# Performance work log

Hardware: AMD Instinct MI355X
Metric: run time of the kernel (lower is better)

Reference implementation:

```python
import jax, jax.numpy as jnp
import numpy as np
import hashlib, struct

TABLE_SIZE = 4_194_304
K_DIM = 8
BATCH = 131_072


def _sha_indices(residues_np: np.ndarray, salt: bytes, table_size: int) -> np.ndarray:
    # Faithful to HeritableTrustVault._hash: clamp, *100, int16 bytes, sha256(salt+bytes),
    # little-endian uint64 of first 8 digest bytes, mod table_size.
    q = (np.clip(residues_np, -30000.0, 30000.0) * 100.0).astype(np.int16)
    out = np.empty(q.shape[0], dtype=np.int64)
    for i in range(q.shape[0]):
        d = hashlib.sha256(salt + q[i].tobytes()).digest()
        out[i] = struct.unpack_from('<Q', d)[0] % table_size
    return out


def setup_inputs() -> dict:
    key = jax.random.key(0)
    k0, k1, k2, k3 = jax.random.split(key, 4)
    residues = jax.random.normal(k0, (BATCH, K_DIM), dtype=jnp.float32)
    survivorship = jax.random.uniform(k1, (BATCH,), dtype=jnp.float32)
    trust_table = jax.random.normal(k2, (TABLE_SIZE, K_DIM), dtype=jnp.float32)
    trust_scores = jax.random.uniform(k3, (TABLE_SIZE,), dtype=jnp.float32)
    longevity = jnp.zeros((TABLE_SIZE,), dtype=jnp.int32)
    salt = np.random.RandomState(0).randint(0, 256, 16, dtype=np.uint8).tobytes()
    indices = jnp.asarray(_sha_indices(np.asarray(residues), salt, TABLE_SIZE))
    return {
        'residues': residues,
        'survivorship': survivorship,
        'trust_table': trust_table,
        'trust_scores': trust_scores,
        'longevity': longevity,
        'indices': indices,
    }


def reference(residues, survivorship, trust_table, trust_scores, longevity, indices):
    # update(): serial compare-exchange loop semantics, vectorized.
    # Final score per slot = max(old_score, max survivorship hashing to it).
    # Winner row per slot = FIRST row with survivorship strictly > old score and
    # equal to the final score (strict '>' means later ties never overwrite).
    B = residues.shape[0]
    T = trust_scores.shape[0]
    old_at = trust_scores[indices]                                  # [B]
    new_scores = trust_scores.at[indices].max(survivorship)         # [T]
    final_at = new_scores[indices]                                  # [B]
    win = (survivorship > old_at) & (survivorship >= final_at)      # [B]
    rows = jnp.arange(B, dtype=jnp.int32)
    cand = jnp.where(win, rows, B)                                  # sentinel B = no winner
    min_row = jnp.full((T,), B, dtype=jnp.int32).at[indices].min(cand)
    has_winner = min_row < B                                        # [T]
    safe_row = jnp.where(has_winner, min_row, 0)
    new_table = jnp.where(has_winner[:, None], residues[safe_row], trust_table)
    new_longevity = longevity.at[indices].add(1)
    # query() after update
    query_scores = new_scores[indices]                              # [B]
    return query_scores, new_table, new_scores, new_longevity
```

## Files before the change

### kernel.cpp

```cpp
#include <hip/hip_runtime.h>

#define T_SIZE 4194304
#define B_SIZE 131072
#define KD 8

__global__ void vault_init_kernel(const float* __restrict__ trust_scores,
                                  const int* __restrict__ longevity,
                                  float* __restrict__ new_scores,
                                  float* __restrict__ new_longevity,
                                  int* __restrict__ min_row) {
    int t = blockIdx.x * blockDim.x + threadIdx.x;
    if (t < T_SIZE / 4) {
        float4 s = ((const float4*)trust_scores)[t];
        int4 l = ((const int4*)longevity)[t];
        float4 lf = make_float4((float)l.x, (float)l.y, (float)l.z, (float)l.w);
        ((float4*)new_scores)[t] = s;
        ((float4*)new_longevity)[t] = lf;
        ((int4*)min_row)[t] = make_int4(B_SIZE, B_SIZE, B_SIZE, B_SIZE);
    }
}

__global__ void vault_scatter_kernel(const float* __restrict__ survivorship,
                                     const int* __restrict__ indices,
                                     float* __restrict__ new_scores,
                                     float* __restrict__ new_longevity) {
    int i = blockIdx.x * blockDim.x + threadIdx.x;
    if (i < B_SIZE) {
        int idx = indices[i];
        atomicMax((int*)(new_scores + idx), __float_as_int(survivorship[i]));
        atomicAdd(new_longevity + idx, 1.0f);
    }
}

__global__ void vault_winner_kernel(const float* __restrict__ survivorship,
                                    const int* __restrict__ indices,
                                    const float* __restrict__ trust_scores,
                                    const float* __restrict__ new_scores,
                                    float* __restrict__ query_scores,
                                    int* __restrict__ min_row) {
    int i = blockIdx.x * blockDim.x + threadIdx.x;
    if (i < B_SIZE) {
        int idx = indices[i];
        float s = survivorship[i];
        float oldv = trust_scores[idx];
        float finalv = new_scores[idx];
        query_scores[i] = finalv;
        if (s > oldv && s >= finalv) {
            atomicMin(min_row + idx, i);
        }
    }
}

__global__ void vault_table_kernel(const float* __restrict__ residues,
                                   const float* __restrict__ trust_table,
                                   const int* __restrict__ min_row,
                                   float* __restrict__ new_table) {
    int t = blockIdx.x * blockDim.x + threadIdx.x;
    if (t < T_SIZE) {
        int r = min_row[t];
        const float4* src = (r < B_SIZE)
            ? (const float4*)(residues + (size_t)r * KD)
            : (const float4*)(trust_table + (size_t)t * KD);
        float4 a = src[0];
        float4 b = src[1];
        float4* dst = (float4*)(new_table + (size_t)t * KD);
        dst[0] = a;
        dst[1] = b;
    }
}

extern "C" void kernel_launch(void* const* d_in, const int* in_sizes, int n_in,
                              void* d_out, int out_size, void* d_ws, size_t ws_size,
                              hipStream_t stream) {
    const float* residues      = (const float*)d_in[0];
    const float* survivorship  = (const float*)d_in[1];
    const float* trust_table   = (const float*)d_in[2];
    const float* trust_scores  = (const float*)d_in[3];
    const int*   longevity     = (const int*)d_in[4];
    const int*   indices       = (const int*)d_in[5];

    float* query_scores  = (float*)d_out;
    float* new_table     = query_scores + B_SIZE;
    float* new_scores    = new_table + (size_t)T_SIZE * KD;
    float* new_longevity = new_scores + T_SIZE;

    int* min_row = (int*)d_ws;

    const int blk = 256;

    vault_init_kernel<<<(T_SIZE / 4 + blk - 1) / blk, blk, 0, stream>>>(
        trust_scores, longevity, new_scores, new_longevity, min_row);

    vault_scatter_kernel<<<(B_SIZE + blk - 1) / blk, blk, 0, stream>>>(
        survivorship, indices, new_scores, new_longevity);

    vault_winner_kernel<<<(B_SIZE + blk - 1) / blk, blk, 0, stream>>>(
        survivorship, indices, trust_scores, new_scores, query_scores, min_row);

    vault_table_kernel<<<(T_SIZE + blk - 1) / blk, blk, 0, stream>>>(
        residues, trust_table, min_row, new_table);
}
```

Before: 320.5 us.

## Pack score and row into a 64-bit atomicMax and fuse finalize kernels

Replaces the separate max-score scatter and min-row winner pass with a single 64-bit atomicMax per row. The key packs the score bits in the high word and the inverted row index in the low word, so the first row holding the max score wins ties. The winner pass and table-copy pass are merged into one finalize kernel that also writes new_scores and query_scores, which removes one launch and one read-modify pass over the slot arrays. The cost is a 32 MB packed workspace in place of a 16 MB min_row buffer. Correctness relies on survivorship being non-negative, so the float bits order like unsigned integers, and on zero-initialised packed words never beating the old score.

```diff
diff --git a/kernel.cpp b/kernel.cpp
--- a/kernel.cpp
+++ b/kernel.cpp
@@ -3,69 +3,67 @@
 #define T_SIZE 4194304
 #define B_SIZE 131072
 #define KD 8
+#define ROW_BLOCKS (B_SIZE / 256)
+#define SLOT_BLOCKS (T_SIZE / 256)
 
-__global__ void vault_init_kernel(const float* __restrict__ trust_scores,
-                                  const int* __restrict__ longevity,
-                                  float* __restrict__ new_scores,
+typedef unsigned long long u64;
+typedef unsigned int u32;
+
+__global__ void vault_init_kernel(const int* __restrict__ longevity,
                                   float* __restrict__ new_longevity,
-                                  int* __restrict__ min_row) {
+                                  u64* __restrict__ packed) {
     int t = blockIdx.x * blockDim.x + threadIdx.x;
-    if (t < T_SIZE / 4) {
-        float4 s = ((const float4*)trust_scores)[t];
-        int4 l = ((const int4*)longevity)[t];
-        float4 lf = make_float4((float)l.x, (float)l.y, (float)l.z, (float)l.w);
-        ((float4*)new_scores)[t] = s;
-        ((float4*)new_longevity)[t] = lf;
-        ((int4*)min_row)[t] = make_int4(B_SIZE, B_SIZE, B_SIZE, B_SIZE);
-    }
+    ulonglong2 z = {0ull, 0ull};
+    ((ulonglong2*)packed)[2 * t]     = z;
+    ((ulonglong2*)packed)[2 * t + 1] = z;
+    int4 l = ((const int4*)longevity)[t];
+    ((float4*)new_longevity)[t] =
+        make_float4((float)l.x, (float)l.y, (float)l.z, (float)l.w);
 }
 
 __global__ void vault_scatter_kernel(const float* __restrict__ survivorship,
                                      const int* __restrict__ indices,
-                                     float* __restrict__ new_scores,
+                                     u64* __restrict__ packed,
                                      float* __restrict__ new_longevity) {
     int i = blockIdx.x * blockDim.x + threadIdx.x;
-    if (i < B_SIZE) {
-        int idx = indices[i];
-        atomicMax((int*)(new_scores + idx), __float_as_int(survivorship[i]));
-        atomicAdd(new_longevity + idx, 1.0f);
-    }
+    int idx = indices[i];
+    u32 bits = __float_as_uint(survivorship[i]);
+    u64 p = ((u64)bits << 32) | (u64)(~(u32)i);
+    atomicMax(packed + idx, p);
+    atomicAdd(new_longevity + idx, 1.0f);
 }
 
-__global__ void vault_winner_kernel(const float* __restrict__ survivorship,
-                                    const int* __restrict__ indices,
-                                    const float* __restrict__ trust_scores,
-                                    const float* __restrict__ new_scores,
-                                    float* __restrict__ query_scores,
-                                    int* __restrict__ min_row) {
-    int i = blockIdx.x * blockDim.x + threadIdx.x;
-    if (i < B_SIZE) {
+__global__ void vault_finalize_kernel(const float* __restrict__ residues,
+                                      const float* __restrict__ trust_table,
+                                      const float* __restrict__ trust_scores,
+                                      const int* __restrict__ indices,
+                                      const u64* __restrict__ packed,
+                                      float* __restrict__ query_scores,
+                                      float* __restrict__ new_table,
+                                      float* __restrict__ new_scores) {
+    int b = blockIdx.x;
+    if (b < ROW_BLOCKS) {
+        int i = b * 256 + threadIdx.x;
         int idx = indices[i];
-        float s = survivorship[i];
+        u64 p = packed[idx];
+        float ms = __uint_as_float((u32)(p >> 32));
         float oldv = trust_scores[idx];
-        float finalv = new_scores[idx];
-        query_scores[i] = finalv;
-        if (s > oldv && s >= finalv) {
-            atomicMin(min_row + idx, i);
-        }
-    }
-}
-
-__global__ void vault_table_kernel(const float* __restrict__ residues,
-                                   const float* __restrict__ trust_table,
-                                   const int* __restrict__ min_row,
-                                   float* __restrict__ new_table) {
-    int t = blockIdx.x * blockDim.x + threadIdx.x;
-    if (t < T_SIZE) {
-        int r = min_row[t];
-        const float4* src = (r < B_SIZE)
+        query_scores[i] = fmaxf(oldv, ms);
+    } else {
+        int t = (b - ROW_BLOCKS) * 256 + threadIdx.x;
+        u64 p = packed[t];
+        float ms = __uint_as_float((u32)(p >> 32));
+        float oldv = trust_scores[t];
+        new_scores[t] = fmaxf(oldv, ms);
+        int r = (int)(~(u32)p);
+        const float4* src = (ms > oldv)
             ? (const float4*)(residues + (size_t)r * KD)
             : (const float4*)(trust_table + (size_t)t * KD);
         float4 a = src[0];
-        float4 b = src[1];
+        float4 c = src[1];
         float4* dst = (float4*)(new_table + (size_t)t * KD);
         dst[0] = a;
-        dst[1] = b;
+        dst[1] = c;
     }
 }
 
@@ -84,19 +82,17 @@
     float* new_scores    = new_table + (size_t)T_SIZE * KD;
     float* new_longevity = new_scores + T_SIZE;
 
-    int* min_row = (int*)d_ws;
+    u64* packed = (u64*)d_ws;
 
     const int blk = 256;
 
-    vault_init_kernel<<<(T_SIZE / 4 + blk - 1) / blk, blk, 0, stream>>>(
-        trust_scores, longevity, new_scores, new_longevity, min_row);
+    vault_init_kernel<<<T_SIZE / 4 / blk, blk, 0, stream>>>(
+        longevity, new_longevity, packed);
 
-    vault_scatter_kernel<<<(B_SIZE + blk - 1) / blk, blk, 0, stream>>>(
-        survivorship, indices, new_scores, new_longevity);
+    vault_scatter_kernel<<<B_SIZE / blk, blk, 0, stream>>>(
+        survivorship, indices, packed, new_longevity);
 
-    vault_winner_kernel<<<(B_SIZE + blk - 1) / blk, blk, 0, stream>>>(
-        survivorship, indices, trust_scores, new_scores, query_scores, min_row);
-
-    vault_table_kernel<<<(T_SIZE + blk - 1) / blk, blk, 0, stream>>>(
-        residues, trust_table, min_row, new_table);
+    vault_finalize_kernel<<<ROW_BLOCKS + SLOT_BLOCKS, blk, 0, stream>>>(
+        residues, trust_table, trust_scores, indices, packed,
+        query_scores, new_table, new_scores);
 }
```

New measurement: 315.3 us. Within noise of the previous version (-1.6%).
